# Optimization experiments

Measured on AMD Instinct MI355X. Metric: run time of the kernel, lower is better.

Reference implementation:

```python
import jax, jax.numpy as jnp
import numpy as np

N_NODES = 50000
N_EDGES = 800000
N_GRAPHS = 64
IN_DIM = 128
HID = 32
HEADS = 4
EDGE_DIM = 8
OUT = 10


def setup_inputs() -> dict:
    key = jax.random.key(0)
    ks = jax.random.split(key, 20)
    s = 0.1
    inp = {
        "x": jax.random.normal(ks[0], (N_NODES, IN_DIM), jnp.float32),
        "edge_index": jax.random.randint(ks[1], (2, N_EDGES), 0, N_NODES, jnp.int32),
        "edge_attr": jax.random.normal(ks[2], (N_EDGES, EDGE_DIM), jnp.float32),
        "batch": jnp.sort(jax.random.randint(ks[3], (N_NODES,), 0, N_GRAPHS, jnp.int32)),
        # conv1: heads=4, out=32
        "W1": jax.random.normal(ks[4], (IN_DIM, HEADS * HID), jnp.float32) * s,
        "att_src1": jax.random.normal(ks[5], (HEADS, HID), jnp.float32) * s,
        "att_dst1": jax.random.normal(ks[6], (HEADS, HID), jnp.float32) * s,
        "We1": jax.random.normal(ks[7], (EDGE_DIM, HEADS * HID), jnp.float32) * s,
        "att_e1": jax.random.normal(ks[8], (HEADS, HID), jnp.float32) * s,
        "b1": jnp.zeros((HEADS * HID,), jnp.float32),
        # conv2: heads=1, out=32
        "W2": jax.random.normal(ks[9], (HEADS * HID, HID), jnp.float32) * s,
        "att_src2": jax.random.normal(ks[10], (1, HID), jnp.float32) * s,
        "att_dst2": jax.random.normal(ks[11], (1, HID), jnp.float32) * s,
        "We2": jax.random.normal(ks[12], (EDGE_DIM, HID), jnp.float32) * s,
        "att_e2": jax.random.normal(ks[13], (1, HID), jnp.float32) * s,
        "b2": jnp.zeros((HID,), jnp.float32),
        # MLP head
        "W3": jax.random.normal(ks[14], (HID, HID // 2), jnp.float32) * s,
        "b3": jnp.zeros((HID // 2,), jnp.float32),
        "W4": jax.random.normal(ks[15], (HID // 2, OUT), jnp.float32) * s,
        "b4": jnp.zeros((OUT,), jnp.float32),
    }
    return inp


def _gat_conv(x, src, dst, eattr, W, a_s, a_d, We, a_e, b, H, C, N):
    """PyG GATConv math (self-loops already appended to src/dst/eattr)."""
    h = (x @ W).reshape(-1, H, C)            # [N,H,C]
    e = (eattr @ We).reshape(-1, H, C)       # [E,H,C]
    al_s = jnp.sum(h * a_s, -1)              # [N,H]
    al_d = jnp.sum(h * a_d, -1)              # [N,H]
    alpha = al_s[src] + al_d[dst] + jnp.sum(e * a_e, -1)   # [E,H]
    alpha = jax.nn.leaky_relu(alpha, 0.2)
    # segment softmax over incoming edges of each dst node
    m = jax.ops.segment_max(alpha, dst, num_segments=N)
    ealpha = jnp.exp(alpha - m[dst])
    denom = jax.ops.segment_sum(ealpha, dst, num_segments=N)
    ealpha = ealpha / (denom[dst] + 1e-16)
    msg = h[src] * ealpha[:, :, None]        # [E,H,C]
    out = jax.ops.segment_sum(msg, dst, num_segments=N)  # [N,H,C]
    return out.reshape(N, H * C) + b


def _forward(x, edge_index, edge_attr, batch,
             W1, att_src1, att_dst1, We1, att_e1, b1,
             W2, att_src2, att_dst2, We2, att_e2, b2,
             W3, b3, W4, b4):
    N = x.shape[0]
    src, dst = edge_index[0], edge_index[1]
    # add_self_loops with fill_value='mean': loop attr = mean of incoming edge_attr
    cnt = jax.ops.segment_sum(jnp.ones((src.shape[0],), x.dtype), dst, num_segments=N)
    loop_attr = jax.ops.segment_sum(edge_attr, dst, num_segments=N) / jnp.maximum(cnt, 1.0)[:, None]
    ar = jnp.arange(N, dtype=src.dtype)
    src2 = jnp.concatenate([src, ar])
    dst2 = jnp.concatenate([dst, ar])
    eattr2 = jnp.concatenate([edge_attr, loop_attr], axis=0)

    h = _gat_conv(x, src2, dst2, eattr2, W1, att_src1, att_dst1, We1, att_e1, b1, HEADS, HID, N)
    h = jax.nn.elu(h)
    h = _gat_conv(h, src2, dst2, eattr2, W2, att_src2, att_dst2, We2, att_e2, b2, 1, HID, N)
    h = jax.nn.elu(h)
    # global mean pool per graph
    gsum = jax.ops.segment_sum(h, batch, num_segments=N_GRAPHS)
    gcnt = jax.ops.segment_sum(jnp.ones((N,), h.dtype), batch, num_segments=N_GRAPHS)
    g = gsum / jnp.maximum(gcnt, 1.0)[:, None]
    # MLP head (eval mode: dropout is identity)
    z = jax.nn.relu(g @ W3 + b3)
    return z @ W4 + b4


def reference(x, edge_index, edge_attr, batch,
              W1, att_src1, att_dst1, We1, att_e1, b1,
              W2, att_src2, att_dst2, We2, att_e2, b2,
              W3, b3, W4, b4):
    return _forward(x, edge_index, edge_attr, batch,
                    W1, att_src1, att_dst1, We1, att_e1, b1,
                    W2, att_src2, att_dst2, We2, att_e2, b2,
                    W3, b3, W4, b4)
```

## Files before the change

kernel.cpp:

```cpp
#include <hip/hip_runtime.h>
#include <hip/hip_bf16.h>
#include <math.h>

#define N_NODES 50000
#define N_EDGES 800000
#define N_GRAPHS 64
#define IN_DIM 128
#define HID 32
#define HEADS 4
#define EDGE_DIM 8
#define OUT_DIM 10
#define HC 128
#define NB 196
#define G1TOT 1563
#define K1GRID 4689
#define EBLK 3125

__device__ __forceinline__ float leaky(float x){ return x >= 0.f ? x : 0.2f*x; }
__device__ __forceinline__ float elu_f(float x){ return x > 0.f ? x : __expf(x)-1.f; }

__device__ __forceinline__ float bf2f(unsigned short u){
  union { unsigned int i; float f; } v; v.i = ((unsigned int)u) << 16; return v.f;
}
__device__ __forceinline__ float lo16(unsigned int u){
  union { unsigned int i; float f; } v; v.i = u << 16; return v.f;
}
__device__ __forceinline__ float hi16(unsigned int u){
  union { unsigned int i; float f; } v; v.i = u & 0xffff0000u; return v.f;
}
__device__ __forceinline__ unsigned short f2bf(float f){
  union { float f; unsigned int i; } v; v.f = f;
  unsigned int r = v.i + 0x7FFF + ((v.i >> 16) & 1);
  return (unsigned short)(r >> 16);
}

__device__ __forceinline__ void gemm1_body(int bb, float* xs, float* ws,
    const float* __restrict__ x, const float* __restrict__ W1,
    const float* __restrict__ as1, const float* __restrict__ ad1,
    unsigned short* __restrict__ h1b, float* __restrict__ als1, float* __restrict__ ald1){
  int t = threadIdx.x;
  int cg = t & 15, c8 = cg*8, qb = (t >> 4)*2;
  int base = bb * 32;
  for (int i = t; i < 1024; i += 256){
    int node = base + (i >> 5);
    int col = (i & 31) * 4;
    float4 v = make_float4(0,0,0,0);
    if (node < N_NODES) v = *(const float4*)&x[node*IN_DIM + col];
    *(float4*)&xs[(i>>5)*128 + col] = v;
  }
  float acc[2][8];
  #pragma unroll
  for (int q = 0; q < 2; q++)
    #pragma unroll
    for (int i = 0; i < 8; i++) acc[q][i] = 0.f;

  for (int kb = 0; kb < 128; kb += 32){
    __syncthreads();
    for (int i = t; i < 1024; i += 256)
      *(float4*)&ws[i*4] = *(const float4*)&W1[kb*128 + i*4];
    __syncthreads();
    #pragma unroll 8
    for (int k = 0; k < 32; k++){
      float4 w0 = *(float4*)&ws[k*128 + c8];
      float4 w1 = *(float4*)&ws[k*128 + c8 + 4];
      #pragma unroll
      for (int q = 0; q < 2; q++){
        float xv = xs[(qb + q)*128 + kb + k];
        acc[q][0] = fmaf(xv, w0.x, acc[q][0]);
        acc[q][1] = fmaf(xv, w0.y, acc[q][1]);
        acc[q][2] = fmaf(xv, w0.z, acc[q][2]);
        acc[q][3] = fmaf(xv, w0.w, acc[q][3]);
        acc[q][4] = fmaf(xv, w1.x, acc[q][4]);
        acc[q][5] = fmaf(xv, w1.y, acc[q][5]);
        acc[q][6] = fmaf(xv, w1.z, acc[q][6]);
        acc[q][7] = fmaf(xv, w1.w, acc[q][7]);
      }
    }
  }
  int head = cg >> 2;
  float asv[8], adv[8];
  #pragma unroll
  for (int i = 0; i < 8; i++){ asv[i] = as1[c8 + i]; adv[i] = ad1[c8 + i]; }
  #pragma unroll
  for (int q = 0; q < 2; q++){
    int n = base + qb + q;
    if (n >= N_NODES) continue;
    float sa = 0.f, sd = 0.f;
    #pragma unroll
    for (int i = 0; i < 8; i++){
      sa = fmaf(acc[q][i], asv[i], sa);
      sd = fmaf(acc[q][i], adv[i], sd);
    }
    sa += __shfl_xor(sa, 1); sd += __shfl_xor(sd, 1);
    sa += __shfl_xor(sa, 2); sd += __shfl_xor(sd, 2);
    uint4 pk;
    pk.x = (unsigned int)f2bf(acc[q][0]) | ((unsigned int)f2bf(acc[q][1]) << 16);
    pk.y = (unsigned int)f2bf(acc[q][2]) | ((unsigned int)f2bf(acc[q][3]) << 16);
    pk.z = (unsigned int)f2bf(acc[q][4]) | ((unsigned int)f2bf(acc[q][5]) << 16);
    pk.w = (unsigned int)f2bf(acc[q][6]) | ((unsigned int)f2bf(acc[q][7]) << 16);
    *(uint4*)&h1b[n*HC + c8] = pk;
    if ((cg & 3) == 0){ als1[n*4 + head] = sa; ald1[n*4 + head] = sd; }
  }
}

__global__ __launch_bounds__(256) void k_f1(const int* __restrict__ dst, const int* __restrict__ src,
    int* __restrict__ cnt, int* __restrict__ rank,
    const float* __restrict__ eattr,
    const float* __restrict__ We1, const float* __restrict__ ae1w,
    const float* __restrict__ We2, const float* __restrict__ ae2w,
    int4* __restrict__ pay,
    const float* __restrict__ x, const float* __restrict__ W1,
    const float* __restrict__ as1, const float* __restrict__ ad1,
    unsigned short* __restrict__ h1b, float* __restrict__ als1, float* __restrict__ ald1){
  __shared__ float smem[8192];
  int m = blockIdx.x % 3, r = blockIdx.x / 3;
  int t = threadIdx.x;
  if (m < 2){
    if (t < 32){
      int d = t >> 2, h = t & 3;
      float s = 0.f;
      for (int c = 0; c < 32; c++) s = fmaf(We1[d*128 + h*32 + c], ae1w[h*32 + c], s);
      smem[d*4 + h] = s;
    } else if (t < 40){
      int d = t - 32;
      float s = 0.f;
      for (int c = 0; c < 32; c++) s = fmaf(We2[d*32 + c], ae2w[c], s);
      smem[32 + d] = s;
    }
    __syncthreads();
    int e = (r*2 + m)*256 + t;
    if (e >= N_EDGES) return;
    int d = dst[e];
    rank[e] = atomicAdd(&cnt[d], 1);
    float4 x0 = *(const float4*)&eattr[(size_t)e*8];
    float4 x1 = *(const float4*)&eattr[(size_t)e*8 + 4];
    float ea[8] = {x0.x,x0.y,x0.z,x0.w,x1.x,x1.y,x1.z,x1.w};
    float4 rr = make_float4(0,0,0,0);
    float r2 = 0.f;
    #pragma unroll
    for (int dd = 0; dd < 8; dd++){
      rr.x = fmaf(ea[dd], smem[dd*4+0], rr.x);
      rr.y = fmaf(ea[dd], smem[dd*4+1], rr.y);
      rr.z = fmaf(ea[dd], smem[dd*4+2], rr.z);
      rr.w = fmaf(ea[dd], smem[dd*4+3], rr.w);
      r2   = fmaf(ea[dd], smem[32+dd], r2);
    }
    int4 rv;
    rv.x = src[e];
    rv.y = (int)((unsigned int)f2bf(rr.x) | ((unsigned int)f2bf(rr.y) << 16));
    rv.z = (int)((unsigned int)f2bf(rr.z) | ((unsigned int)f2bf(rr.w) << 16));
    rv.w = __float_as_int(r2);
    pay[e] = rv;
    return;
  }
  gemm1_body(r, smem, smem + 4096, x, W1, as1, ad1, h1b, als1, ald1);
}

__global__ __launch_bounds__(256) void k_blocksum(const int* __restrict__ cnt, int* __restrict__ bsum){
  __shared__ int sh[256];
  int n = blockIdx.x*256 + threadIdx.x;
  sh[threadIdx.x] = (n < N_NODES) ? cnt[n] : 0;
  __syncthreads();
  for (int off = 128; off > 0; off >>= 1){
    if (threadIdx.x < off) sh[threadIdx.x] += sh[threadIdx.x + off];
    __syncthreads();
  }
  if (threadIdx.x == 0) bsum[blockIdx.x] = sh[0];
}

__global__ __launch_bounds__(256) void k_scanb(const int* __restrict__ bsum, int* __restrict__ bpre){
  __shared__ int sh[256];
  int t = threadIdx.x;
  int v = (t < NB) ? bsum[t] : 0;
  sh[t] = v; __syncthreads();
  for (int off = 1; off < 256; off <<= 1){
    int u = (t >= off) ? sh[t-off] : 0;
    __syncthreads();
    sh[t] += u;
    __syncthreads();
  }
  if (t < NB) bpre[t] = sh[t] - v;
}

__global__ __launch_bounds__(256) void k_rowptr(const int* __restrict__ cnt, const int* __restrict__ bpre,
    int* __restrict__ rowptr){
  __shared__ int sh[256];
  int t = threadIdx.x; int n = blockIdx.x*256 + t;
  int c = (n < N_NODES) ? cnt[n] : 0;
  sh[t] = c; __syncthreads();
  for (int off = 1; off < 256; off <<= 1){
    int u = (t >= off) ? sh[t-off] : 0;
    __syncthreads();
    sh[t] += u;
    __syncthreads();
  }
  int incl = sh[t];
  if (n < N_NODES){
    rowptr[n] = bpre[blockIdx.x] + incl - c;
  }
  if (n == N_NODES-1) rowptr[N_NODES] = bpre[blockIdx.x] + incl;
}

__global__ __launch_bounds__(256) void k_f2(const int* __restrict__ dst,
    const int* __restrict__ rank, const int* __restrict__ rowptr,
    const int4* __restrict__ pay, int4* __restrict__ rec){
  int e = blockIdx.x*256 + threadIdx.x;
  if (e >= N_EDGES) return;
  int d = dst[e];
  int rk = rank[e];
  int4 rv = pay[e];
  rec[rowptr[d] + rk] = rv;
}

__global__ __launch_bounds__(256) void k_conv1(const int* __restrict__ rowptr, const int4* __restrict__ rec,
    const float* __restrict__ als1, const float* __restrict__ ald1,
    const unsigned short* __restrict__ h1b, const float* __restrict__ b1,
    const float* __restrict__ W2, const float* __restrict__ as2, const float* __restrict__ ad2,
    unsigned short* __restrict__ h2b, float* __restrict__ als2, float* __restrict__ ald2){
  __shared__ float oex[4][128];
  int wv = threadIdx.x >> 6, l = threadIdx.x & 63;
  int n = blockIdx.x*4 + wv;
  int g = l >> 4, il = l & 15;
  int c0 = il*8, h = il >> 2;
  int hs1 = (h & 1) * 16;
  float ad = ald1[n*4 + h];
  float den = 0.f, sum_ae = 0.f;
  float acc[8];
  #pragma unroll
  for (int i = 0; i < 8; i++) acc[i] = 0.f;
  int r0 = rowptr[n], r1 = rowptr[n+1];
  for (int k = r0 + g; k < r1; k += 4){
    int4 q = rec[k];
    unsigned int w = (h & 2) ? (unsigned int)q.z : (unsigned int)q.y;
    float aev = bf2f((unsigned short)(w >> hs1));
    float as_v = als1[q.x*4 + h];
    uint4 hv = *(const uint4*)(h1b + q.x*HC + c0);
    float p = __expf(leaky(as_v + ad + aev));
    sum_ae += aev; den += p;
    acc[0] = fmaf(p, lo16(hv.x), acc[0]);
    acc[1] = fmaf(p, hi16(hv.x), acc[1]);
    acc[2] = fmaf(p, lo16(hv.y), acc[2]);
    acc[3] = fmaf(p, hi16(hv.y), acc[3]);
    acc[4] = fmaf(p, lo16(hv.z), acc[4]);
    acc[5] = fmaf(p, hi16(hv.z), acc[5]);
    acc[6] = fmaf(p, lo16(hv.w), acc[6]);
    acc[7] = fmaf(p, hi16(hv.w), acc[7]);
  }
  #pragma unroll
  for (int off = 16; off < 64; off <<= 1){
    den    += __shfl_xor(den, off);
    sum_ae += __shfl_xor(sum_ae, off);
    #pragma unroll
    for (int i = 0; i < 8; i++) acc[i] += __shfl_xor(acc[i], off);
  }
  int cn = r1 - r0; if (cn < 1) cn = 1;
  float ps = __expf(leaky(als1[n*4 + h] + ad + sum_ae / (float)cn));
  uint4 hs = *(const uint4*)(h1b + n*HC + c0);
  den += ps;
  acc[0] = fmaf(ps, lo16(hs.x), acc[0]);
  acc[1] = fmaf(ps, hi16(hs.x), acc[1]);
  acc[2] = fmaf(ps, lo16(hs.y), acc[2]);
  acc[3] = fmaf(ps, hi16(hs.y), acc[3]);
  acc[4] = fmaf(ps, lo16(hs.z), acc[4]);
  acc[5] = fmaf(ps, hi16(hs.z), acc[5]);
  acc[6] = fmaf(ps, lo16(hs.w), acc[6]);
  acc[7] = fmaf(ps, hi16(hs.w), acc[7]);
  float inv = 1.f / (den + 1e-16f);
  float4 bv0 = *(const float4*)&b1[c0];
  float4 bv1 = *(const float4*)&b1[c0 + 4];
  float o0 = elu_f(fmaf(acc[0], inv, bv0.x));
  float o1 = elu_f(fmaf(acc[1], inv, bv0.y));
  float o2 = elu_f(fmaf(acc[2], inv, bv0.z));
  float o3 = elu_f(fmaf(acc[3], inv, bv0.w));
  float o4 = elu_f(fmaf(acc[4], inv, bv1.x));
  float o5 = elu_f(fmaf(acc[5], inv, bv1.y));
  float o6 = elu_f(fmaf(acc[6], inv, bv1.z));
  float o7 = elu_f(fmaf(acc[7], inv, bv1.w));
  float* op = oex[wv];
  if (g == 0){
    *(float4*)&op[c0]     = make_float4(o0, o1, o2, o3);
    *(float4*)&op[c0 + 4] = make_float4(o4, o5, o6, o7);
  }
  __syncthreads();
  int j = l & 31, hf = l >> 5;
  int cb = hf * 64;
  float s = 0.f;
  #pragma unroll 8
  for (int c = 0; c < 64; c++)
    s = fmaf(op[cb + c], W2[(cb + c)*32 + j], s);
  s += __shfl_xor(s, 32);
  float sa = s * as2[j], sd = s * ad2[j];
  #pragma unroll
  for (int off = 1; off < 32; off <<= 1){
    sa += __shfl_xor(sa, off); sd += __shfl_xor(sd, off);
  }
  if (l < 32) h2b[n*32 + j] = f2bf(s);
  if (l == 0){ als2[n] = sa; ald2[n] = sd; }
}

__global__ __launch_bounds__(256) void k_conv2(const int* __restrict__ rowptr, const int4* __restrict__ rec,
    const float* __restrict__ als2, const float* __restrict__ ald2,
    const unsigned short* __restrict__ h2b, const float* __restrict__ b2, float* __restrict__ out2){
  int wv = threadIdx.x >> 6, l = threadIdx.x & 63;
  int n = blockIdx.x*4 + wv;
  if (n >= N_NODES) return;
  int g = l >> 3, il = l & 7;
  int c0 = il*4;
  float ad = ald2[n];
  float den = 0.f, sum_ae = 0.f;
  float acc[4];
  #pragma unroll
  for (int i = 0; i < 4; i++) acc[i] = 0.f;
  int r0 = rowptr[n], r1 = rowptr[n+1];
  for (int k = r0 + g; k < r1; k += 8){
    int4 q = rec[k];
    float aev = __int_as_float(q.w);
    float as_v = als2[q.x];
    uint2 hv = *(const uint2*)(h2b + q.x*32 + c0);
    float p = __expf(leaky(as_v + ad + aev));
    sum_ae += aev; den += p;
    acc[0] = fmaf(p, lo16(hv.x), acc[0]);
    acc[1] = fmaf(p, hi16(hv.x), acc[1]);
    acc[2] = fmaf(p, lo16(hv.y), acc[2]);
    acc[3] = fmaf(p, hi16(hv.y), acc[3]);
  }
  #pragma unroll
  for (int off = 8; off < 64; off <<= 1){
    den    += __shfl_xor(den, off);
    sum_ae += __shfl_xor(sum_ae, off);
    #pragma unroll
    for (int i = 0; i < 4; i++) acc[i] += __shfl_xor(acc[i], off);
  }
  int cn = r1 - r0; if (cn < 1) cn = 1;
  float ps = __expf(leaky(als2[n] + ad + sum_ae / (float)cn));
  uint2 hs = *(const uint2*)(h2b + n*32 + c0);
  den += ps;
  acc[0] = fmaf(ps, lo16(hs.x), acc[0]);
  acc[1] = fmaf(ps, hi16(hs.x), acc[1]);
  acc[2] = fmaf(ps, lo16(hs.y), acc[2]);
  acc[3] = fmaf(ps, hi16(hs.y), acc[3]);
  float inv = 1.f / (den + 1e-16f);
  float4 bv = *(const float4*)&b2[c0];
  if (g == 0){
    float4 ov;
    ov.x = elu_f(fmaf(acc[0], inv, bv.x));
    ov.y = elu_f(fmaf(acc[1], inv, bv.y));
    ov.z = elu_f(fmaf(acc[2], inv, bv.z));
    ov.w = elu_f(fmaf(acc[3], inv, bv.w));
    *(float4*)&out2[n*32 + c0] = ov;
  }
}

__global__ __launch_bounds__(256) void k_pool(const float* __restrict__ out2, const int* __restrict__ batch,
    float* __restrict__ gpool){
  int g = blockIdx.x;
  int a = 0, b = N_NODES;
  while (a < b){ int mid = (a + b) >> 1; if (batch[mid] < g) a = mid + 1; else b = mid; }
  int lo = a;
  a = lo; b = N_NODES;
  while (a < b){ int mid = (a + b) >> 1; if (batch[mid] < g + 1) a = mid + 1; else b = mid; }
  int hi = a;
  int t = threadIdx.x, c = t & 31, r = t >> 5;
  float s = 0.f;
  for (int n = lo + r; n < hi; n += 8) s += out2[n*32 + c];
  __shared__ float sh[256];
  sh[t] = s; __syncthreads();
  if (r == 0){
    for (int q = 1; q < 8; q++) s += sh[q*32 + c];
    int cg = hi - lo; if (cg < 1) cg = 1;
    gpool[g*32 + c] = s / (float)cg;
  }
}

__global__ __launch_bounds__(1024) void k_mlp(const float* __restrict__ gpool, const float* __restrict__ W3,
    const float* __restrict__ b3, const float* __restrict__ W4, const float* __restrict__ b4,
    float* __restrict__ out){
  __shared__ float z[64*16];
  int t = threadIdx.x;
  {
    int g = t >> 4, jj = t & 15;
    float s = b3[jj];
    #pragma unroll
    for (int c = 0; c < 32; c++) s = fmaf(gpool[g*32 + c], W3[c*16 + jj], s);
    z[t] = fmaxf(s, 0.f);
  }
  __syncthreads();
  if (t < 640){
    int g = t / 10, o = t - g*10;
    float s = b4[o];
    #pragma unroll
    for (int jj = 0; jj < 16; jj++) s = fmaf(z[g*16 + jj], W4[jj*10 + o], s);
    out[t] = s;
  }
}

extern "C" void kernel_launch(void* const* d_in, const int* in_sizes, int n_in,
                              void* d_out, int out_size, void* d_ws, size_t ws_size,
                              hipStream_t stream) {
  (void)in_sizes; (void)n_in; (void)out_size; (void)ws_size;
  const float* x     = (const float*)d_in[0];
  const int*   ei    = (const int*)  d_in[1];
  const float* eattr = (const float*)d_in[2];
  const int*   batch = (const int*)  d_in[3];
  const float* W1    = (const float*)d_in[4];
  const float* as1   = (const float*)d_in[5];
  const float* ad1   = (const float*)d_in[6];
  const float* We1   = (const float*)d_in[7];
  const float* ae1w  = (const float*)d_in[8];
  const float* b1    = (const float*)d_in[9];
  const float* W2    = (const float*)d_in[10];
  const float* as2   = (const float*)d_in[11];
  const float* ad2   = (const float*)d_in[12];
  const float* We2   = (const float*)d_in[13];
  const float* ae2w  = (const float*)d_in[14];
  const float* b2    = (const float*)d_in[15];
  const float* W3    = (const float*)d_in[16];
  const float* b3    = (const float*)d_in[17];
  const float* W4    = (const float*)d_in[18];
  const float* b4    = (const float*)d_in[19];
  float* out = (float*)d_out;
  const int* src  = ei;
  const int* dstp = ei + N_EDGES;

  char* p = (char*)d_ws;
  auto alloc = [&](size_t bytes)->void*{ void* r = (void*)p; p += (bytes + 255) & ~(size_t)255; return r; };
  int*    cnt      = (int*)   alloc(4*N_NODES);
  size_t  zero_bytes = (size_t)(p - (char*)d_ws);
  int*    rank     = (int*)   alloc(4*N_EDGES);
  int*    rowptr   = (int*)   alloc(4*(N_NODES+1));
  int*    bsum     = (int*)   alloc(4*NB);
  int*    bpre     = (int*)   alloc(4*NB);
  int4*   pay      = (int4*)  alloc(16*N_EDGES);
  int4*   rec      = (int4*)  alloc(16*N_EDGES);
  unsigned short* h1b  = (unsigned short*)alloc(2*N_NODES*HC);
  float*  als1     = (float*) alloc(16*N_NODES);
  float*  ald1     = (float*) alloc(16*N_NODES);
  unsigned short* h2b  = (unsigned short*)alloc(2*N_NODES*HID);
  float*  als2     = (float*) alloc(4*N_NODES);
  float*  ald2     = (float*) alloc(4*N_NODES);
  float*  out2     = (float*) alloc(4*N_NODES*HID);
  float*  gpool    = (float*) alloc(4*N_GRAPHS*HID);

  hipMemsetAsync(d_ws, 0, zero_bytes, stream);
  k_f1      <<<K1GRID, 256, 0, stream>>>(dstp, src, cnt, rank, eattr, We1, ae1w, We2, ae2w,
                                         pay, x, W1, as1, ad1, h1b, als1, ald1);
  k_blocksum<<<NB,    256, 0, stream>>>(cnt, bsum);
  k_scanb   <<<1,     256, 0, stream>>>(bsum, bpre);
  k_rowptr  <<<NB,    256, 0, stream>>>(cnt, bpre, rowptr);
  k_f2      <<<EBLK,  256, 0, stream>>>(dstp, rank, rowptr, pay, rec);
  k_conv1   <<<N_NODES/4, 256, 0, stream>>>(rowptr, rec, als1, ald1, h1b, b1,
                                            W2, as2, ad2, h2b, als2, ald2);
  k_conv2   <<<(N_NODES+3)/4, 256, 0, stream>>>(rowptr, rec, als2, ald2, h2b, b2, out2);
  k_pool    <<<N_GRAPHS, 256, 0, stream>>>(out2, batch, gpool);
  k_mlp     <<<1,    1024, 0, stream>>>(gpool, W3, b3, W4, b4, out);
}
```

Baseline: 322.5 us.

## Scatter edge indices instead of payload records and unroll gather loops by two

The CSR build now scatters only a 4-byte edge index per edge instead of copying the 16-byte payload record into sorted order. Both conv kernels then read the payload indirectly through that index. The conv gather loops are also unrolled to process two edges per iteration, which raises memory-level parallelism. This cuts scatter write traffic, but the conv kernels now make an extra dependent, uncoalesced random read of the payload for each edge, in both conv1 and conv2.

```diff
diff --git a/kernel.cpp b/kernel.cpp
--- a/kernel.cpp
+++ b/kernel.cpp
@@ -203,16 +203,14 @@
 
 __global__ __launch_bounds__(256) void k_f2(const int* __restrict__ dst,
     const int* __restrict__ rank, const int* __restrict__ rowptr,
-    const int4* __restrict__ pay, int4* __restrict__ rec){
+    int* __restrict__ eidx){
   int e = blockIdx.x*256 + threadIdx.x;
   if (e >= N_EDGES) return;
-  int d = dst[e];
-  int rk = rank[e];
-  int4 rv = pay[e];
-  rec[rowptr[d] + rk] = rv;
-}
-
-__global__ __launch_bounds__(256) void k_conv1(const int* __restrict__ rowptr, const int4* __restrict__ rec,
+  eidx[rowptr[dst[e]] + rank[e]] = e;
+}
+
+__global__ __launch_bounds__(256) void k_conv1(const int* __restrict__ rowptr, const int* __restrict__ eidx,
+    const int4* __restrict__ pay,
     const float* __restrict__ als1, const float* __restrict__ ald1,
     const unsigned short* __restrict__ h1b, const float* __restrict__ b1,
     const float* __restrict__ W2, const float* __restrict__ as2, const float* __restrict__ ad2,
@@ -229,8 +227,33 @@
   #pragma unroll
   for (int i = 0; i < 8; i++) acc[i] = 0.f;
   int r0 = rowptr[n], r1 = rowptr[n+1];
-  for (int k = r0 + g; k < r1; k += 4){
-    int4 q = rec[k];
+  int k = r0 + g;
+  for (; k + 4 < r1; k += 8){
+    int e0 = eidx[k], e1 = eidx[k+4];
+    int4 q0 = pay[e0], q1 = pay[e1];
+    unsigned int w0 = (h & 2) ? (unsigned int)q0.z : (unsigned int)q0.y;
+    unsigned int w1 = (h & 2) ? (unsigned int)q1.z : (unsigned int)q1.y;
+    float ae0 = bf2f((unsigned short)(w0 >> hs1));
+    float ae1v = bf2f((unsigned short)(w1 >> hs1));
+    float as0 = als1[q0.x*4 + h], as1v = als1[q1.x*4 + h];
+    uint4 hv0 = *(const uint4*)(h1b + q0.x*HC + c0);
+    uint4 hv1 = *(const uint4*)(h1b + q1.x*HC + c0);
+    float p0 = __expf(leaky(as0 + ad + ae0));
+    float p1 = __expf(leaky(as1v + ad + ae1v));
+    sum_ae += ae0 + ae1v;
+    den += p0 + p1;
+    acc[0] = fmaf(p0, lo16(hv0.x), acc[0]); acc[0] = fmaf(p1, lo16(hv1.x), acc[0]);
+    acc[1] = fmaf(p0, hi16(hv0.x), acc[1]); acc[1] = fmaf(p1, hi16(hv1.x), acc[1]);
+    acc[2] = fmaf(p0, lo16(hv0.y), acc[2]); acc[2] = fmaf(p1, lo16(hv1.y), acc[2]);
+    acc[3] = fmaf(p0, hi16(hv0.y), acc[3]); acc[3] = fmaf(p1, hi16(hv1.y), acc[3]);
+    acc[4] = fmaf(p0, lo16(hv0.z), acc[4]); acc[4] = fmaf(p1, lo16(hv1.z), acc[4]);
+    acc[5] = fmaf(p0, hi16(hv0.z), acc[5]); acc[5] = fmaf(p1, hi16(hv1.z), acc[5]);
+    acc[6] = fmaf(p0, lo16(hv0.w), acc[6]); acc[6] = fmaf(p1, lo16(hv1.w), acc[6]);
+    acc[7] = fmaf(p0, hi16(hv0.w), acc[7]); acc[7] = fmaf(p1, hi16(hv1.w), acc[7]);
+  }
+  if (k < r1){
+    int e0 = eidx[k];
+    int4 q = pay[e0];
     unsigned int w = (h & 2) ? (unsigned int)q.z : (unsigned int)q.y;
     float aev = bf2f((unsigned short)(w >> hs1));
     float as_v = als1[q.x*4 + h];
@@ -298,7 +321,8 @@
   if (l == 0){ als2[n] = sa; ald2[n] = sd; }
 }
 
-__global__ __launch_bounds__(256) void k_conv2(const int* __restrict__ rowptr, const int4* __restrict__ rec,
+__global__ __launch_bounds__(256) void k_conv2(const int* __restrict__ rowptr, const int* __restrict__ eidx,
+    const int4* __restrict__ pay,
     const float* __restrict__ als2, const float* __restrict__ ald2,
     const unsigned short* __restrict__ h2b, const float* __restrict__ b2, float* __restrict__ out2){
   int wv = threadIdx.x >> 6, l = threadIdx.x & 63;
@@ -312,12 +336,29 @@
   #pragma unroll
   for (int i = 0; i < 4; i++) acc[i] = 0.f;
   int r0 = rowptr[n], r1 = rowptr[n+1];
-  for (int k = r0 + g; k < r1; k += 8){
-    int4 q = rec[k];
+  int k = r0 + g;
+  for (; k + 8 < r1; k += 16){
+    int e0 = eidx[k], e1 = eidx[k+8];
+    int4 q0 = pay[e0], q1 = pay[e1];
+    float ae0 = __int_as_float(q0.w), ae1v = __int_as_float(q1.w);
+    float as0 = als2[q0.x], as1v = als2[q1.x];
+    uint2 hv0 = *(const uint2*)(h2b + q0.x*32 + c0);
+    uint2 hv1 = *(const uint2*)(h2b + q1.x*32 + c0);
+    float p0 = __expf(leaky(as0 + ad + ae0));
+    float p1 = __expf(leaky(as1v + ad + ae1v));
+    sum_ae += ae0 + ae1v;
+    den += p0 + p1;
+    acc[0] = fmaf(p0, lo16(hv0.x), acc[0]); acc[0] = fmaf(p1, lo16(hv1.x), acc[0]);
+    acc[1] = fmaf(p0, hi16(hv0.x), acc[1]); acc[1] = fmaf(p1, hi16(hv1.x), acc[1]);
+    acc[2] = fmaf(p0, lo16(hv0.y), acc[2]); acc[2] = fmaf(p1, lo16(hv1.y), acc[2]);
+    acc[3] = fmaf(p0, hi16(hv0.y), acc[3]); acc[3] = fmaf(p1, hi16(hv1.y), acc[3]);
+  }
+  if (k < r1){
+    int e0 = eidx[k];
+    int4 q = pay[e0];
     float aev = __int_as_float(q.w);
-    float as_v = als2[q.x];
+    float p = __expf(leaky(als2[q.x] + ad + aev));
     uint2 hv = *(const uint2*)(h2b + q.x*32 + c0);
-    float p = __expf(leaky(as_v + ad + aev));
     sum_ae += aev; den += p;
     acc[0] = fmaf(p, lo16(hv.x), acc[0]);
     acc[1] = fmaf(p, hi16(hv.x), acc[1]);
@@ -431,7 +472,7 @@
   int*    bsum     = (int*)   alloc(4*NB);
   int*    bpre     = (int*)   alloc(4*NB);
   int4*   pay      = (int4*)  alloc(16*N_EDGES);
-  int4*   rec      = (int4*)  alloc(16*N_EDGES);
+  int*    eidx     = (int*)   alloc(4*N_EDGES);
   unsigned short* h1b  = (unsigned short*)alloc(2*N_NODES*HC);
   float*  als1     = (float*) alloc(16*N_NODES);
   float*  ald1     = (float*) alloc(16*N_NODES);
@@ -447,10 +488,10 @@
   k_blocksum<<<NB,    256, 0, stream>>>(cnt, bsum);
   k_scanb   <<<1,     256, 0, stream>>>(bsum, bpre);
   k_rowptr  <<<NB,    256, 0, stream>>>(cnt, bpre, rowptr);
-  k_f2      <<<EBLK,  256, 0, stream>>>(dstp, rank, rowptr, pay, rec);
-  k_conv1   <<<N_NODES/4, 256, 0, stream>>>(rowptr, rec, als1, ald1, h1b, b1,
+  k_f2      <<<EBLK,  256, 0, stream>>>(dstp, rank, rowptr, eidx);
+  k_conv1   <<<N_NODES/4, 256, 0, stream>>>(rowptr, eidx, pay, als1, ald1, h1b, b1,
                                             W2, as2, ad2, h2b, als2, ald2);
-  k_conv2   <<<(N_NODES+3)/4, 256, 0, stream>>>(rowptr, rec, als2, ald2, h2b, b2, out2);
+  k_conv2   <<<(N_NODES+3)/4, 256, 0, stream>>>(rowptr, eidx, pay, als2, ald2, h2b, b2, out2);
   k_pool    <<<N_GRAPHS, 256, 0, stream>>>(out2, batch, gpool);
   k_mlp     <<<1,    1024, 0, stream>>>(gpool, W3, b3, W4, b4, out);
 }
```

New measurement: 329.9 us. 1.02x slower.
